# Kernel optimization log

Hardware: AMD Instinct MI355X
Metric: run time of the kernel (lower is better)

## Reference

```python
import jax, jax.numpy as jnp
import numpy as np

NUM_USERS, NUM_ITEMS, D = 100000, 200000, 128
B, LLEN, SLEN = 4096, 200, 50
NEG = -1e9


def setup_inputs() -> dict:
    key = jax.random.key(0)
    ks = jax.random.split(key, 10)
    w_range = float(np.sqrt(3.0 / D))
    return {
        "user_table": 0.01 * jax.random.normal(ks[0], (NUM_USERS, D), dtype=jnp.float32),
        "item_table": 0.01 * jax.random.normal(ks[1], (NUM_ITEMS, D), dtype=jnp.float32),
        "W1": jax.random.uniform(ks[2], (2 * D, 16), minval=-w_range, maxval=w_range, dtype=jnp.float32),
        "b1": jnp.zeros((16,), dtype=jnp.float32),
        "W2": jax.random.uniform(ks[3], (16, 1), minval=-w_range, maxval=w_range, dtype=jnp.float32),
        "b2": jnp.zeros((1,), dtype=jnp.float32),
        "user_inputs": jax.random.randint(ks[4], (B,), 0, NUM_USERS, dtype=jnp.int64) if jax.config.jax_enable_x64 else jax.random.randint(ks[4], (B,), 0, NUM_USERS, dtype=jnp.int32),
        "L_inputs": jax.random.randint(ks[5], (B, LLEN), 0, NUM_ITEMS, dtype=jnp.int32),
        "S_inputs": jax.random.randint(ks[6], (B, SLEN), 0, NUM_ITEMS, dtype=jnp.int32),
        "item_inputs": jax.random.randint(ks[7], (B,), 0, NUM_ITEMS, dtype=jnp.int32),
    }


def reference(user_table, item_table, W1, b1, W2, b2,
              user_inputs, L_inputs, S_inputs, item_inputs):
    def att_logits(x):  # x: [..., 2D] -> [...]
        h = jax.nn.relu(x @ W1 + b1)
        return (h @ W2 + b2)[..., 0]

    def masked_softmax(logits, mask):  # softmax over last axis restricted to mask
        logits = jnp.where(mask, logits, NEG)
        return jax.nn.softmax(logits, axis=-1)

    u_emb = user_table[user_inputs]                      # [B, D]

    # ---- long-term attention over L history ----
    L_mask = L_inputs >= 0                               # [B, L]
    L_idx = jnp.where(L_mask, L_inputs, 0)
    L_emb = item_table[L_idx]                            # [B, L, D]
    uL = jnp.concatenate([jnp.broadcast_to(u_emb[:, None, :], L_emb.shape), L_emb], axis=-1)  # [B, L, 2D]
    w1 = masked_softmax(att_logits(uL), L_mask)          # [B, L]
    u_long = jnp.einsum('bl,bld->bd', w1, L_emb)         # [B, D]

    # ---- short-term attention over [u_long] + S (L assumed nonempty) ----
    S_mask = S_inputs >= 0                               # [B, S]
    S_idx = jnp.where(S_mask, S_inputs, 0)
    S_emb = item_table[S_idx]                            # [B, S, D]
    seq = jnp.concatenate([u_long[:, None, :], S_emb], axis=1)   # [B, 1+S, D]
    seq_mask = jnp.concatenate([jnp.ones((seq.shape[0], 1), dtype=bool), S_mask], axis=1)
    uSeq = jnp.concatenate([jnp.broadcast_to(u_emb[:, None, :], seq.shape), seq], axis=-1)  # [B, 1+S, 2D]
    w2 = masked_softmax(att_logits(uSeq), seq_mask)      # [B, 1+S]
    user_hybrid = jnp.einsum('bs,bsd->bd', w2, seq)      # [B, D]

    # ---- score: bmm([B,1,D], [B,D,1]) -> [B,1,1] ----
    item_emb = item_table[item_inputs]                   # [B, D]
    score = jnp.sum(user_hybrid * item_emb, axis=-1)[:, None, None]
    return score
```

## Files before the change

### kernel.cpp

```cpp
#include <hip/hip_runtime.h>
#include <math.h>

#define D 128
#define LLEN 200
#define SLEN 50
#define CH 64
#define ESTR 129
#define NEG (-1e9f)

__device__ __forceinline__ float wave_red_sum(float v) {
#pragma unroll
  for (int m = 32; m >= 1; m >>= 1) v += __shfl_xor(v, m, 64);
  return v;
}
__device__ __forceinline__ float block_sum(float v, float* red) {
  v = wave_red_sum(v);
  if ((threadIdx.x & 63) == 0) red[threadIdx.x >> 6] = v;
  __syncthreads();
  v = red[0] + red[1] + red[2] + red[3];
  __syncthreads();
  return v;
}

__global__ void __launch_bounds__(256, 4) din_kernel(
    const float* __restrict__ user_table, const float* __restrict__ item_table,
    const float* __restrict__ W1, const float* __restrict__ b1,
    const float* __restrict__ W2, const float* __restrict__ b2,
    const int* __restrict__ user_inputs, const int* __restrict__ L_inputs,
    const int* __restrict__ S_inputs, const int* __restrict__ item_inputs,
    float* __restrict__ out) {
  __shared__ float ebuf[CH * ESTR];
  __shared__ float hspart[4 * 65];
  __shared__ float w_sh[CH];
  __shared__ int rows1[LLEN];
  __shared__ int rowsS[SLEN];
  __shared__ float upart_sh[16];
  __shared__ float red_sh[4];

  const int b = blockIdx.x;
  const int tid = threadIdx.x;
  const int lane = tid & 63;
  const int w = __builtin_amdgcn_readfirstlane(tid >> 6);
  const int dd = tid & 127, dg = tid >> 7;
  const float4* it4 = reinterpret_cast<const float4*>(item_table);

  float* u_sh = &ebuf[0];
  float* part = &ebuf[128];
  if (tid < D) u_sh[tid] = user_table[(size_t)user_inputs[b] * D + tid];
  if (tid < LLEN) rows1[tid] = L_inputs[(size_t)b * LLEN + tid];
  if (tid < SLEN) rowsS[tid] = S_inputs[(size_t)b * SLEN + tid];
  __syncthreads();

  {
    int j = tid & 15, g = tid >> 4;
    float p = 0.f;
#pragma unroll
    for (int t = 0; t < 8; ++t) {
      int d = g * 8 + t;
      p = fmaf(u_sh[d], W1[d * 16 + j], p);
    }
    part[tid] = p;
  }
  __syncthreads();
  if (tid < 16) {
    float s = b1[tid];
#pragma unroll
    for (int g = 0; g < 16; ++g) s += part[g * 16 + tid];
    upart_sh[tid] = s;
  }
  __syncthreads();

  const float b2v = b2[0];
  const float w2a = W2[4 * w + 0], w2b = W2[4 * w + 1];
  const float w2c = W2[4 * w + 2], w2d = W2[4 * w + 3];

  float pacc = 0.f;
  float uacc = 0.f;

  for (int c = 0; c < 4; ++c) {
    const int base = c * CH;
    const int cnt = (base + CH <= LLEN) ? CH : (LLEN - base);
    const int nslot = cnt * 32;

    {
      float4 v[8];
#pragma unroll
      for (int it = 0; it < 8; ++it) {
        int s = tid + it * 256;
        if (s < nslot) {
          int gid = rows1[base + (s >> 5)];
          if (gid < 0) gid = 0;
          v[it] = it4[(size_t)gid * 32 + (s & 31)];
        }
      }
#pragma unroll
      for (int it = 0; it < 8; ++it) {
        int s = tid + it * 256;
        if (s < nslot) {
          float* dst = &ebuf[(s >> 5) * ESTR + 4 * (s & 31)];
          dst[0] = v[it].x; dst[1] = v[it].y; dst[2] = v[it].z; dst[3] = v[it].w;
        }
      }
    }
    __syncthreads();

    if (lane < cnt) {
      float a0 = 0.f, a1 = 0.f, a2 = 0.f, a3 = 0.f;
      const float* er = &ebuf[lane * ESTR];
      const float* wc = &W1[(size_t)D * 16 + 4 * w];
#pragma unroll 16
      for (int d = 0; d < D; ++d) {
        float e = er[d];
        const float* wr = wc + d * 16;
        a0 = fmaf(e, wr[0], a0);
        a1 = fmaf(e, wr[1], a1);
        a2 = fmaf(e, wr[2], a2);
        a3 = fmaf(e, wr[3], a3);
      }
      float hs = fmaxf(upart_sh[4 * w + 0] + a0, 0.f) * w2a;
      hs = fmaf(fmaxf(upart_sh[4 * w + 1] + a1, 0.f), w2b, hs);
      hs = fmaf(fmaxf(upart_sh[4 * w + 2] + a2, 0.f), w2c, hs);
      hs = fmaf(fmaxf(upart_sh[4 * w + 3] + a3, 0.f), w2d, hs);
      hspart[w * 65 + lane] = hs;
    }
    __syncthreads();

    if (tid < cnt) {
      float lg = hspart[tid] + hspart[65 + tid] + hspart[130 + tid] +
                 hspart[195 + tid] + b2v;
      float p = (rows1[base + tid] >= 0) ? expf(lg) : 0.f;
      w_sh[tid] = p;
      pacc += p;
    }
    __syncthreads();

    for (int l = dg; l < cnt; l += 2)
      uacc = fmaf(w_sh[l], ebuf[l * ESTR + dd], uacc);
    __syncthreads();
  }

  const float invS1 = 1.f / block_sum(pacc, red_sh);
  float* part2 = &ebuf[60 * ESTR];
  part2[tid] = uacc;
  __syncthreads();
  if (tid < D) {
    float ul = (part2[tid] + part2[tid + D]) * invS1;
    ebuf[tid] = ul;
  }
  __syncthreads();

  {
    const int nslot = SLEN * 32;
    float4 v[7];
#pragma unroll
    for (int it = 0; it < 7; ++it) {
      int s = tid + it * 256;
      if (s < nslot) {
        int gid = rowsS[s >> 5];
        if (gid < 0) gid = 0;
        v[it] = it4[(size_t)gid * 32 + (s & 31)];
      }
    }
#pragma unroll
    for (int it = 0; it < 7; ++it) {
      int s = tid + it * 256;
      if (s < nslot) {
        float* dst = &ebuf[((s >> 5) + 1) * ESTR + 4 * (s & 31)];
        dst[0] = v[it].x; dst[1] = v[it].y; dst[2] = v[it].z; dst[3] = v[it].w;
      }
    }
  }
  __syncthreads();

  const int n2 = 1 + SLEN;
  if (lane < n2) {
    float a0 = 0.f, a1 = 0.f, a2 = 0.f, a3 = 0.f;
    const float* er = &ebuf[lane * ESTR];
    const float* wc = &W1[(size_t)D * 16 + 4 * w];
#pragma unroll 16
    for (int d = 0; d < D; ++d) {
      float e = er[d];
      const float* wr = wc + d * 16;
      a0 = fmaf(e, wr[0], a0);
      a1 = fmaf(e, wr[1], a1);
      a2 = fmaf(e, wr[2], a2);
      a3 = fmaf(e, wr[3], a3);
    }
    float hs = fmaxf(upart_sh[4 * w + 0] + a0, 0.f) * w2a;
    hs = fmaf(fmaxf(upart_sh[4 * w + 1] + a1, 0.f), w2b, hs);
    hs = fmaf(fmaxf(upart_sh[4 * w + 2] + a2, 0.f), w2c, hs);
    hs = fmaf(fmaxf(upart_sh[4 * w + 3] + a3, 0.f), w2d, hs);
    hspart[w * 65 + lane] = hs;
  }
  __syncthreads();

  float p2 = 0.f;
  if (tid < n2) {
    float lg = hspart[tid] + hspart[65 + tid] + hspart[130 + tid] +
               hspart[195 + tid] + b2v;
    bool valid = (tid == 0) || (rowsS[tid - 1] >= 0);
    p2 = valid ? expf(lg) : 0.f;
    w_sh[tid] = p2;
  }
  const float invS2 = 1.f / block_sum(p2, red_sh);

  float uacc2 = 0.f;
  for (int l = dg; l < n2; l += 2)
    uacc2 = fmaf(w_sh[l], ebuf[l * ESTR + dd], uacc2);
  part2[tid] = uacc2;
  __syncthreads();

  float sv = 0.f;
  if (tid < D) {
    float uh = (part2[tid] + part2[tid + D]) * invS2;
    sv = uh * item_table[(size_t)item_inputs[b] * D + tid];
  }
  float tot = block_sum(sv, red_sh);
  if (tid == 0) out[b] = tot;
}

extern "C" void kernel_launch(void* const* d_in, const int* in_sizes, int n_in,
                              void* d_out, int out_size, void* d_ws, size_t ws_size,
                              hipStream_t stream) {
  const float* user_table = (const float*)d_in[0];
  const float* item_table = (const float*)d_in[1];
  const float* W1 = (const float*)d_in[2];
  const float* b1 = (const float*)d_in[3];
  const float* W2 = (const float*)d_in[4];
  const float* b2 = (const float*)d_in[5];
  const int* user_inputs = (const int*)d_in[6];
  const int* L_inputs = (const int*)d_in[7];
  const int* S_inputs = (const int*)d_in[8];
  const int* item_inputs = (const int*)d_in[9];
  float* out = (float*)d_out;

  const int B = in_sizes[6];
  din_kernel<<<B, 256, 0, stream>>>(user_table, item_table, W1, b1, W2, b2,
                                    user_inputs, L_inputs, S_inputs, item_inputs,
                                    out);
}
```

Measured before the change: 297.8 us.

## Prefetch next history chunk into registers and vectorize LDS accesses with float4

Issues the gather for the first L chunk before computing the user projection, and in each chunk iteration loads the next chunk (or the S items on the last iteration) into registers while the current chunk is being scored. This hides global gather latency behind compute. The LDS row stride is padded to 132 so that float4 stores and loads of embedding rows are aligned. The MLP and weighted-sum loops now read float4 from shared memory, and the weighted sum uses 8 row groups with float4 accumulators. The cost is higher register pressure and possible LDS bank conflicts from the new stride.

```diff
diff --git a/kernel.cpp b/kernel.cpp
--- a/kernel.cpp
+++ b/kernel.cpp
@@ -5,7 +5,7 @@
 #define LLEN 200
 #define SLEN 50
 #define CH 64
-#define ESTR 129
+#define ESTR 132
 #define NEG (-1e9f)
 
 __device__ __forceinline__ float wave_red_sum(float v) {
@@ -29,7 +29,7 @@
     const int* __restrict__ user_inputs, const int* __restrict__ L_inputs,
     const int* __restrict__ S_inputs, const int* __restrict__ item_inputs,
     float* __restrict__ out) {
-  __shared__ float ebuf[CH * ESTR];
+  __shared__ __align__(16) float ebuf[CH * ESTR];
   __shared__ float hspart[4 * 65];
   __shared__ float w_sh[CH];
   __shared__ int rows1[LLEN];
@@ -41,7 +41,7 @@
   const int tid = threadIdx.x;
   const int lane = tid & 63;
   const int w = __builtin_amdgcn_readfirstlane(tid >> 6);
-  const int dd = tid & 127, dg = tid >> 7;
+  const int q = tid & 31, g = tid >> 5;
   const float4* it4 = reinterpret_cast<const float4*>(item_table);
 
   float* u_sh = &ebuf[0];
@@ -51,12 +51,21 @@
   if (tid < SLEN) rowsS[tid] = S_inputs[(size_t)b * SLEN + tid];
   __syncthreads();
 
+  float4 v[8];
+#pragma unroll
+  for (int it = 0; it < 8; ++it) {
+    int s = tid + it * 256;
+    int gid = rows1[s >> 5];
+    if (gid < 0) gid = 0;
+    v[it] = it4[(size_t)gid * 32 + (s & 31)];
+  }
+
   {
-    int j = tid & 15, g = tid >> 4;
+    int j = tid & 15, gg = tid >> 4;
     float p = 0.f;
 #pragma unroll
     for (int t = 0; t < 8; ++t) {
-      int d = g * 8 + t;
+      int d = gg * 8 + t;
       p = fmaf(u_sh[d], W1[d * 16 + j], p);
     }
     part[tid] = p;
@@ -65,7 +74,7 @@
   if (tid < 16) {
     float s = b1[tid];
 #pragma unroll
-    for (int g = 0; g < 16; ++g) s += part[g * 16 + tid];
+    for (int gg = 0; gg < 16; ++gg) s += part[gg * 16 + tid];
     upart_sh[tid] = s;
   }
   __syncthreads();
@@ -75,47 +84,61 @@
   const float w2c = W2[4 * w + 2], w2d = W2[4 * w + 3];
 
   float pacc = 0.f;
-  float uacc = 0.f;
+  float4 uacc = make_float4(0.f, 0.f, 0.f, 0.f);
 
   for (int c = 0; c < 4; ++c) {
     const int base = c * CH;
     const int cnt = (base + CH <= LLEN) ? CH : (LLEN - base);
     const int nslot = cnt * 32;
 
-    {
-      float4 v[8];
+#pragma unroll
+    for (int it = 0; it < 8; ++it) {
+      int s = tid + it * 256;
+      if (s < nslot)
+        *reinterpret_cast<float4*>(&ebuf[(s >> 5) * ESTR + 4 * (s & 31)]) = v[it];
+    }
+    __syncthreads();
+
+    if (c < 3) {
+      const int nbase = (c + 1) * CH;
+      const int nn = ((nbase + CH <= LLEN) ? CH : (LLEN - nbase)) * 32;
 #pragma unroll
       for (int it = 0; it < 8; ++it) {
         int s = tid + it * 256;
-        if (s < nslot) {
-          int gid = rows1[base + (s >> 5)];
+        if (s < nn) {
+          int gid = rows1[nbase + (s >> 5)];
           if (gid < 0) gid = 0;
           v[it] = it4[(size_t)gid * 32 + (s & 31)];
         }
       }
-#pragma unroll
-      for (int it = 0; it < 8; ++it) {
+    } else {
+#pragma unroll
+      for (int it = 0; it < 7; ++it) {
         int s = tid + it * 256;
-        if (s < nslot) {
-          float* dst = &ebuf[(s >> 5) * ESTR + 4 * (s & 31)];
-          dst[0] = v[it].x; dst[1] = v[it].y; dst[2] = v[it].z; dst[3] = v[it].w;
+        if (s < SLEN * 32) {
+          int gid = rowsS[s >> 5];
+          if (gid < 0) gid = 0;
+          v[it] = it4[(size_t)gid * 32 + (s & 31)];
         }
       }
     }
-    __syncthreads();
 
     if (lane < cnt) {
       float a0 = 0.f, a1 = 0.f, a2 = 0.f, a3 = 0.f;
-      const float* er = &ebuf[lane * ESTR];
+      const float4* er4 = reinterpret_cast<const float4*>(&ebuf[lane * ESTR]);
       const float* wc = &W1[(size_t)D * 16 + 4 * w];
-#pragma unroll 16
-      for (int d = 0; d < D; ++d) {
-        float e = er[d];
-        const float* wr = wc + d * 16;
-        a0 = fmaf(e, wr[0], a0);
-        a1 = fmaf(e, wr[1], a1);
-        a2 = fmaf(e, wr[2], a2);
-        a3 = fmaf(e, wr[3], a3);
+#pragma unroll
+      for (int t = 0; t < 32; ++t) {
+        float4 e = er4[t];
+        const float* wr = wc + (4 * t) * 16;
+        a0 = fmaf(e.x, wr[0], a0);  a1 = fmaf(e.x, wr[1], a1);
+        a2 = fmaf(e.x, wr[2], a2);  a3 = fmaf(e.x, wr[3], a3);
+        a0 = fmaf(e.y, wr[16], a0); a1 = fmaf(e.y, wr[17], a1);
+        a2 = fmaf(e.y, wr[18], a2); a3 = fmaf(e.y, wr[19], a3);
+        a0 = fmaf(e.z, wr[32], a0); a1 = fmaf(e.z, wr[33], a1);
+        a2 = fmaf(e.z, wr[34], a2); a3 = fmaf(e.z, wr[35], a3);
+        a0 = fmaf(e.w, wr[48], a0); a1 = fmaf(e.w, wr[49], a1);
+        a2 = fmaf(e.w, wr[50], a2); a3 = fmaf(e.w, wr[51], a3);
       }
       float hs = fmaxf(upart_sh[4 * w + 0] + a0, 0.f) * w2a;
       hs = fmaf(fmaxf(upart_sh[4 * w + 1] + a1, 0.f), w2b, hs);
@@ -134,57 +157,55 @@
     }
     __syncthreads();
 
-    for (int l = dg; l < cnt; l += 2)
-      uacc = fmaf(w_sh[l], ebuf[l * ESTR + dd], uacc);
-    __syncthreads();
-  }
-
+    for (int l = g; l < cnt; l += 8) {
+      float pw = w_sh[l];
+      float4 e = reinterpret_cast<const float4*>(&ebuf[l * ESTR])[q];
+      uacc.x = fmaf(pw, e.x, uacc.x);
+      uacc.y = fmaf(pw, e.y, uacc.y);
+      uacc.z = fmaf(pw, e.z, uacc.z);
+      uacc.w = fmaf(pw, e.w, uacc.w);
+    }
+    __syncthreads();
+  }
+
+  float4* part4 = reinterpret_cast<float4*>(&ebuf[52 * ESTR]);
+  part4[tid] = uacc;
   const float invS1 = 1.f / block_sum(pacc, red_sh);
-  float* part2 = &ebuf[60 * ESTR];
-  part2[tid] = uacc;
-  __syncthreads();
-  if (tid < D) {
-    float ul = (part2[tid] + part2[tid + D]) * invS1;
-    ebuf[tid] = ul;
-  }
-  __syncthreads();
-
-  {
-    const int nslot = SLEN * 32;
-    float4 v[7];
-#pragma unroll
-    for (int it = 0; it < 7; ++it) {
-      int s = tid + it * 256;
-      if (s < nslot) {
-        int gid = rowsS[s >> 5];
-        if (gid < 0) gid = 0;
-        v[it] = it4[(size_t)gid * 32 + (s & 31)];
-      }
-    }
-#pragma unroll
-    for (int it = 0; it < 7; ++it) {
-      int s = tid + it * 256;
-      if (s < nslot) {
-        float* dst = &ebuf[((s >> 5) + 1) * ESTR + 4 * (s & 31)];
-        dst[0] = v[it].x; dst[1] = v[it].y; dst[2] = v[it].z; dst[3] = v[it].w;
-      }
-    }
+  if (tid < 32) {
+    float4 t = part4[tid];
+#pragma unroll
+    for (int gg = 1; gg < 8; ++gg) {
+      float4 o = part4[gg * 32 + tid];
+      t.x += o.x; t.y += o.y; t.z += o.z; t.w += o.w;
+    }
+    t.x *= invS1; t.y *= invS1; t.z *= invS1; t.w *= invS1;
+    reinterpret_cast<float4*>(ebuf)[tid] = t;
+  }
+#pragma unroll
+  for (int it = 0; it < 7; ++it) {
+    int s = tid + it * 256;
+    if (s < SLEN * 32)
+      *reinterpret_cast<float4*>(&ebuf[((s >> 5) + 1) * ESTR + 4 * (s & 31)]) = v[it];
   }
   __syncthreads();
 
   const int n2 = 1 + SLEN;
   if (lane < n2) {
     float a0 = 0.f, a1 = 0.f, a2 = 0.f, a3 = 0.f;
-    const float* er = &ebuf[lane * ESTR];
+    const float4* er4 = reinterpret_cast<const float4*>(&ebuf[lane * ESTR]);
     const float* wc = &W1[(size_t)D * 16 + 4 * w];
-#pragma unroll 16
-    for (int d = 0; d < D; ++d) {
-      float e = er[d];
-      const float* wr = wc + d * 16;
-      a0 = fmaf(e, wr[0], a0);
-      a1 = fmaf(e, wr[1], a1);
-      a2 = fmaf(e, wr[2], a2);
-      a3 = fmaf(e, wr[3], a3);
+#pragma unroll
+    for (int t = 0; t < 32; ++t) {
+      float4 e = er4[t];
+      const float* wr = wc + (4 * t) * 16;
+      a0 = fmaf(e.x, wr[0], a0);  a1 = fmaf(e.x, wr[1], a1);
+      a2 = fmaf(e.x, wr[2], a2);  a3 = fmaf(e.x, wr[3], a3);
+      a0 = fmaf(e.y, wr[16], a0); a1 = fmaf(e.y, wr[17], a1);
+      a2 = fmaf(e.y, wr[18], a2); a3 = fmaf(e.y, wr[19], a3);
+      a0 = fmaf(e.z, wr[32], a0); a1 = fmaf(e.z, wr[33], a1);
+      a2 = fmaf(e.z, wr[34], a2); a3 = fmaf(e.z, wr[35], a3);
+      a0 = fmaf(e.w, wr[48], a0); a1 = fmaf(e.w, wr[49], a1);
+      a2 = fmaf(e.w, wr[50], a2); a3 = fmaf(e.w, wr[51], a3);
     }
     float hs = fmaxf(upart_sh[4 * w + 0] + a0, 0.f) * w2a;
     hs = fmaf(fmaxf(upart_sh[4 * w + 1] + a1, 0.f), w2b, hs);
@@ -204,16 +225,28 @@
   }
   const float invS2 = 1.f / block_sum(p2, red_sh);
 
-  float uacc2 = 0.f;
-  for (int l = dg; l < n2; l += 2)
-    uacc2 = fmaf(w_sh[l], ebuf[l * ESTR + dd], uacc2);
-  part2[tid] = uacc2;
+  float4 uacc2 = make_float4(0.f, 0.f, 0.f, 0.f);
+  for (int l = g; l < n2; l += 8) {
+    float pw = w_sh[l];
+    float4 e = reinterpret_cast<const float4*>(&ebuf[l * ESTR])[q];
+    uacc2.x = fmaf(pw, e.x, uacc2.x);
+    uacc2.y = fmaf(pw, e.y, uacc2.y);
+    uacc2.z = fmaf(pw, e.z, uacc2.z);
+    uacc2.w = fmaf(pw, e.w, uacc2.w);
+  }
+  part4[tid] = uacc2;
   __syncthreads();
 
   float sv = 0.f;
-  if (tid < D) {
-    float uh = (part2[tid] + part2[tid + D]) * invS2;
-    sv = uh * item_table[(size_t)item_inputs[b] * D + tid];
+  if (tid < 32) {
+    float4 t = part4[tid];
+#pragma unroll
+    for (int gg = 1; gg < 8; ++gg) {
+      float4 o = part4[gg * 32 + tid];
+      t.x += o.x; t.y += o.y; t.z += o.z; t.w += o.w;
+    }
+    float4 iv = it4[(size_t)item_inputs[b] * 32 + tid];
+    sv = (t.x * iv.x + t.y * iv.y + t.z * iv.z + t.w * iv.w) * invS2;
   }
   float tot = block_sum(sv, red_sh);
   if (tid == 0) out[b] = tot;
```

Result: slower. 490.9 us (+64.8%).
